# Optimization experiments

Measured on AMD Instinct MI355X. Metric: run time of the kernel, lower is better.

## Reference

```python
import jax, jax.numpy as jnp
import numpy as np

N, M, H = 200000, 400000, 128
EPS = 1e-12  # torch F.normalize eps


def _l2norm(x):
    # F.normalize(x, p=2, dim=-1): x / max(||x||, eps)
    n = jnp.linalg.norm(x, axis=-1, keepdims=True)
    return x / jnp.maximum(n, EPS)


def message_norm(feat, msg, scale):
    # DGL MessageNorm(learn_scale=True): normalize(msg) * ||feat|| * scale
    feat_norm = jnp.linalg.norm(feat, axis=-1, keepdims=True)
    return _l2norm(msg) * feat_norm * scale


def setup_inputs() -> dict:
    key = jax.random.key(0)
    ks = jax.random.split(key, 8)
    h_src = jax.random.normal(ks[0], (M, H), dtype=jnp.float32)
    c_src = jax.random.normal(ks[1], (M, H), dtype=jnp.float32)
    iou = jax.random.normal(ks[2], (N, 3 * H), dtype=jnp.float32)
    child_idx = jax.random.randint(ks[3], (N, 2), 0, M, dtype=jnp.int64)
    # torch nn.Linear layout: y = x @ W.T + b
    lim_f = 1.0 / np.sqrt(2 * H)
    W_f = jax.random.uniform(ks[4], (2 * H, 2 * H), minval=-lim_f, maxval=lim_f, dtype=jnp.float32)
    b_f = jax.random.uniform(ks[5], (2 * H,), minval=-lim_f, maxval=lim_f, dtype=jnp.float32)
    W_iou = jax.random.uniform(ks[6], (3 * H, 2 * H), minval=-lim_f, maxval=lim_f, dtype=jnp.float32)
    b_iou = jnp.zeros((1, 3 * H), dtype=jnp.float32)
    scale_iou = jnp.ones((), dtype=jnp.float32)
    scale_c = jnp.ones((), dtype=jnp.float32)
    return {"h_src": h_src, "c_src": c_src, "iou": iou, "child_idx": child_idx,
            "W_f": W_f, "b_f": b_f, "W_iou": W_iou, "b_iou": b_iou,
            "scale_iou": scale_iou, "scale_c": scale_c}


def reference(h_src, c_src, iou, child_idx, W_f, b_f, W_iou, b_iou, scale_iou, scale_c):
    # --- reduce_func: gather children, forget gates, weighted cell sum ---
    h_ch = h_src[child_idx]                 # [N, 2, H]
    c_ch = c_src[child_idx]                 # [N, 2, H]
    h_cat = h_ch.reshape(h_ch.shape[0], -1)  # [N, 2H]
    f = jax.nn.sigmoid(h_cat @ W_f.T + b_f).reshape(h_ch.shape)  # [N, 2, H]
    c_sum = jnp.sum(f * c_ch, axis=1)       # [N, H]
    iou_n = message_norm(iou, h_cat, scale_iou) @ W_iou.T  # [N, 3H]
    c_dat = message_norm(c_ch[:, 0, :], c_sum, scale_c)    # [N, H]
    # --- apply_node_func ---
    iou_b = iou_n + b_iou
    i, o, u = jnp.split(iou_b, 3, axis=1)
    c = jax.nn.sigmoid(i) * jnp.tanh(u) + c_dat
    h = jax.nn.sigmoid(o) * jnp.tanh(c)
    return jnp.stack([h, c], axis=1)        # [N, 2, H]
```

## Files before the change

kernel.cpp:

```cpp
#include <hip/hip_runtime.h>
#include <math.h>

typedef __attribute__((ext_vector_type(4))) float f32x4;
typedef __attribute__((ext_vector_type(2))) float f32x2;
typedef __attribute__((ext_vector_type(8))) short bf16x8;
typedef __attribute__((ext_vector_type(4))) short short4v;

#define EPSN 1e-12f
#define TN 32
#define FS 260
#define IS 388
#define FBASE 8192
#define UTOT 16512

__device__ inline short f2bf(float x) {
    union { float f; unsigned u; } v; v.f = x;
    unsigned r = v.u + 0x7fffu + ((v.u >> 16) & 1u);
    return (short)(r >> 16);
}
__device__ inline float bf2f(short s) {
    union { unsigned u; float f; } v;
    v.u = ((unsigned)(unsigned short)s) << 16;
    return v.f;
}
__device__ inline float wsum64(float v) {
#pragma unroll
    for (int m = 32; m > 0; m >>= 1) v += __shfl_xor(v, m);
    return v;
}
__device__ inline float wsum32(float v) {
    v += __shfl_xor(v, 1);
    v += __shfl_xor(v, 2);
    v += __shfl_xor(v, 4);
    v += __shfl_xor(v, 8);
    v += __shfl_xor(v, 16);
    return v;
}
__device__ inline float sigm(float x) { return 1.0f / (1.0f + __expf(-x)); }
__device__ inline float tanh_fast(float x) {
    float a = fabsf(x);
    float e = __expf(2.0f * a);
    float t = 1.0f - 2.0f / (e + 1.0f);
    return copysignf(t, x);
}
__device__ inline float dot4(f32x4 v) { return v.x*v.x + v.y*v.y + v.z*v.z + v.w*v.w; }
__device__ inline short4v pack4(f32x4 v) {
    short4v p;
    p.x = f2bf(v.x); p.y = f2bf(v.y); p.z = f2bf(v.z); p.w = f2bf(v.w);
    return p;
}

__global__ void prep_B(const float* __restrict__ W_f, const float* __restrict__ W_iou,
                       short* __restrict__ Blin) {
    int t = blockIdx.x * 256 + threadIdx.x;
    if (t >= 8 * 40 * 64) return;
    int lane = t & 63;
    int jb = (t >> 6) % 40;
    int kb = (t >> 6) / 40;
    int j = jb * 16 + (lane & 15);
    int k = kb * 32 + ((lane >> 4) << 3);
    const float* src = (j < 256) ? (W_f + (size_t)j * 256 + k)
                                 : (W_iou + (size_t)(j - 256) * 256 + k);
    bf16x8 v;
#pragma unroll
    for (int e = 0; e < 8; ++e) v[e] = f2bf(src[e]);
    *(bf16x8*)(Blin + (size_t)t * 8) = v;
}

template<int NJJ>
__device__ inline void gpass32(const short* __restrict__ A, const short* __restrict__ Blin,
                               int lane, int jbase, f32x4 acc[2][NJJ]) {
    const int la = lane & 15, kg = lane >> 4;
#pragma unroll
    for (int kb = 0; kb < 8; ++kb) {
        bf16x8 af[2];
#pragma unroll
        for (int m = 0; m < 2; ++m) {
            const int f = kb * 128 + kg * 32 + m * 16 + la;
            af[m] = *(const bf16x8*)&A[(f ^ ((f >> 5) & 7)) << 3];
        }
#pragma unroll
        for (int jj = 0; jj < NJJ; ++jj) {
            const bf16x8 b = *(const bf16x8*)(Blin +
                ((size_t)((kb * 40 + jbase + jj) * 64 + lane)) * 8);
            acc[0][jj] = __builtin_amdgcn_mfma_f32_16x16x32_bf16(af[0], b, acc[0][jj], 0, 0, 0);
            acc[1][jj] = __builtin_amdgcn_mfma_f32_16x16x32_bf16(af[1], b, acc[1][jj], 0, 0, 0);
        }
    }
}

__global__ __launch_bounds__(512, 4) void tree_fused(
    const float* __restrict__ h_src, const float* __restrict__ c_src,
    const float* __restrict__ iou, const int* __restrict__ child_idx,
    const float* __restrict__ b_f, const float* __restrict__ b_iou,
    const float* __restrict__ sc_iou_p, const float* __restrict__ sc_c_p,
    const short* __restrict__ Blin, float* __restrict__ out) {
    __shared__ __align__(16) short U[UTOT];
    __shared__ float h_n2[TN], iou_n2[TN];
    __shared__ int cc_lds[TN][2];

    const int tid = threadIdx.x;
    const int wave = tid >> 6;
    const int lane = tid & 63;
    const int la = lane & 15, kg = lane >> 4;
    const size_t nb0 = (size_t)blockIdx.x * TN;

    const float sc_iou = sc_iou_p[0];
    const float sc_c = sc_c_p[0];

    {
        const int child = lane >> 5;
        const int seg = lane & 31;
        int cix[4];
#pragma unroll
        for (int r = 0; r < 4; ++r)
            cix[r] = child_idx[(size_t)(nb0 + wave + 8 * r) * 2 + child];
#pragma unroll
        for (int half = 0; half < 2; ++half) {
            f32x4 hv[2], v4[2];
            f32x2 v2[2];
#pragma unroll
            for (int rr = 0; rr < 2; ++rr) {
                const int r = half * 2 + rr;
                const size_t node = nb0 + wave + 8 * r;
                hv[rr] = *(const f32x4*)(h_src + (size_t)cix[r] * 128 + seg * 4);
                v4[rr] = *(const f32x4*)(iou + node * 384 + lane * 4);
                v2[rr] = *(const f32x2*)(iou + node * 384 + 256 + lane * 2);
            }
#pragma unroll
            for (int rr = 0; rr < 2; ++rr) {
                const int r = half * 2 + rr;
                const int nd = wave + 8 * r;
                const int f = (child * 4 + (seg >> 3)) * 128 + ((seg >> 1) & 3) * 32 + nd;
                const int addr = ((f ^ ((f >> 5) & 7)) << 3) + (seg & 1) * 4;
                short4v a4;
                a4.x = f2bf(hv[rr].x); a4.y = f2bf(hv[rr].y);
                a4.z = f2bf(hv[rr].z); a4.w = f2bf(hv[rr].w);
                *(short4v*)&U[addr] = a4;
                if (lane == 0) cc_lds[nd][0] = cix[r];
                if (lane == 32) cc_lds[nd][1] = cix[r];
                float hss = wsum64(dot4(hv[rr]));
                float iss = wsum64(dot4(v4[rr]) + v2[rr].x * v2[rr].x + v2[rr].y * v2[rr].y);
                if (lane == 0) { h_n2[nd] = hss; iou_n2[nd] = iss; }
            }
            __builtin_amdgcn_sched_barrier(0);
        }
    }
    __syncthreads();

    const int nd0 = tid >> 5;
    const int q = tid & 31;
    const int h0q = q * 4;

    short4v c0a, c1a;
    float n2a;
    {
        const int c00 = cc_lds[nd0][0];
        const int c01 = cc_lds[nd0][1];
        const f32x4 t0 = *(const f32x4*)(c_src + (size_t)c00 * 128 + h0q);
        const f32x4 t1 = *(const f32x4*)(c_src + (size_t)c01 * 128 + h0q);
        n2a = dot4(t0);
        c0a = pack4(t0);
        c1a = pack4(t1);
    }

    {
        f32x4 accf[2][2];
        const float bf0 = b_f[(wave * 2 + 0) * 16 + la];
        const float bf1 = b_f[(wave * 2 + 1) * 16 + la];
        accf[0][0] = (f32x4){bf0, bf0, bf0, bf0};
        accf[1][0] = accf[0][0];
        accf[0][1] = (f32x4){bf1, bf1, bf1, bf1};
        accf[1][1] = accf[0][1];
        gpass32<2>(U, Blin, lane, wave * 2, accf);
#pragma unroll
        for (int m = 0; m < 2; ++m)
#pragma unroll
            for (int jj = 0; jj < 2; ++jj) {
                const int col = (wave * 2 + jj) * 16 + la;
#pragma unroll
                for (int r = 0; r < 4; ++r) {
                    const int row = m * 16 + kg * 4 + r;
                    U[FBASE + row * FS + col] = f2bf(accf[m][jj][r]);
                }
            }
    }

    short4v c0b, c1b;
    float n2b;
    {
        const int c10 = cc_lds[16 + nd0][0];
        const int c11 = cc_lds[16 + nd0][1];
        const f32x4 t0 = *(const f32x4*)(c_src + (size_t)c10 * 128 + h0q);
        const f32x4 t1 = *(const f32x4*)(c_src + (size_t)c11 * 128 + h0q);
        n2b = dot4(t0);
        c0b = pack4(t0);
        c1b = pack4(t1);
    }
    __syncthreads();

    f32x4 accio[2][3];
#pragma unroll
    for (int m = 0; m < 2; ++m)
#pragma unroll
        for (int jj = 0; jj < 3; ++jj) accio[m][jj] = (f32x4){0.f, 0.f, 0.f, 0.f};
    gpass32<3>(U, Blin, lane, 16 + wave * 3, accio);

    float csr[2][4], s_v[2];
#pragma unroll
    for (int p = 0; p < 2; ++p) {
        const int nd = p * 16 + nd0;
        const short4v c0v = p ? c0b : c0a;
        const short4v c1v = p ? c1b : c1a;
        const short4v yf0 = *(const short4v*)&U[FBASE + nd * FS + h0q];
        const short4v yf1 = *(const short4v*)&U[FBASE + nd * FS + 128 + h0q];
        float c0n2 = wsum32(p ? n2b : n2a);
        float cs[4];
        float csn2 = 0.f;
#pragma unroll
        for (int e = 0; e < 4; ++e) {
            const float f0 = sigm(bf2f(yf0[e]));
            const float f1 = sigm(bf2f(yf1[e]));
            const float v = f0 * bf2f(c0v[e]) + f1 * bf2f(c1v[e]);
            cs[e] = v;
            csn2 += v * v;
        }
        csn2 = wsum32(csn2);
        const float rs = sc_c * sqrtf(c0n2) / fmaxf(sqrtf(csn2), EPSN);
#pragma unroll
        for (int e = 0; e < 4; ++e) csr[p][e] = cs[e] * rs;
        s_v[p] = sc_iou * sqrtf(iou_n2[nd]) / fmaxf(sqrtf(h_n2[nd]), EPSN);
    }
    __syncthreads();

#pragma unroll
    for (int m = 0; m < 2; ++m)
#pragma unroll
        for (int jj = 0; jj < 3; ++jj) {
            const int col = (wave * 3 + jj) * 16 + la;
#pragma unroll
            for (int r = 0; r < 4; ++r) {
                const int row = m * 16 + kg * 4 + r;
                U[row * IS + col] = f2bf(accio[m][jj][r]);
            }
        }
    __syncthreads();

    const f32x4 bi0 = *(const f32x4*)(b_iou + h0q);
    const f32x4 bi1 = *(const f32x4*)(b_iou + 128 + h0q);
    const f32x4 bi2 = *(const f32x4*)(b_iou + 256 + h0q);
#pragma unroll
    for (int p = 0; p < 2; ++p) {
        const int nd = p * 16 + nd0;
        const size_t node = nb0 + nd;
        const short4v yi = *(const short4v*)&U[nd * IS + h0q];
        const short4v yo = *(const short4v*)&U[nd * IS + 128 + h0q];
        const short4v yu = *(const short4v*)&U[nd * IS + 256 + h0q];
        f32x4 outh, outc;
#pragma unroll
        for (int e = 0; e < 4; ++e) {
            const float iv = bf2f(yi[e]) * s_v[p] + ((const float*)&bi0)[e];
            const float ov = bf2f(yo[e]) * s_v[p] + ((const float*)&bi1)[e];
            const float uv = bf2f(yu[e]) * s_v[p] + ((const float*)&bi2)[e];
            const float cval = sigm(iv) * tanh_fast(uv) + csr[p][e];
            const float hval = sigm(ov) * tanh_fast(cval);
            ((float*)&outh)[e] = hval;
            ((float*)&outc)[e] = cval;
        }
        *(f32x4*)(out + node * 256 + h0q) = outh;
        *(f32x4*)(out + node * 256 + 128 + h0q) = outc;
    }
}

extern "C" void kernel_launch(void* const* d_in, const int* in_sizes, int n_in,
                              void* d_out, int out_size, void* d_ws, size_t ws_size,
                              hipStream_t stream) {
    const float* h_src = (const float*)d_in[0];
    const float* c_src = (const float*)d_in[1];
    const float* iou = (const float*)d_in[2];
    const int* cidx = (const int*)d_in[3];
    const float* W_f = (const float*)d_in[4];
    const float* b_f = (const float*)d_in[5];
    const float* W_iou = (const float*)d_in[6];
    const float* b_iou = (const float*)d_in[7];
    const float* s_iou = (const float*)d_in[8];
    const float* s_c = (const float*)d_in[9];
    float* out = (float*)d_out;
    short* Blin = (short*)d_ws;

    const int N = in_sizes[3] / 2;
    const int ntiles = N / TN;
    hipLaunchKernelGGL(prep_B, dim3(80), dim3(256), 0, stream, W_f, W_iou, Blin);
    hipLaunchKernelGGL(tree_fused, dim3(ntiles), dim3(512), 0, stream,
                       h_src, c_src, iou, cidx, b_f, b_iou, s_iou, s_c, Blin, out);
}
```

Baseline: 255.2 us.

## Make tree kernel persistent with double-buffered prefetch of next tile's gathers

Converts the one-tile-per-block kernel into a persistent grid-stride loop over 512 blocks, double-buffering the A-operand tile, child indices and norms in LDS. Gathers and norms for the next tile are issued while the current tile's GEMMs and epilogue run, so gather latency overlaps with compute. LDS use grows to about 74 KB per block, which lowers occupancy (the grid is capped at 512 blocks) and adds register pressure from the prefetched values held across the loop.

After: 616.8 us. +141.6%, slower.

```diff
diff --git a/kernel.cpp b/kernel.cpp
--- a/kernel.cpp
+++ b/kernel.cpp
@@ -8,10 +8,13 @@
 
 #define EPSN 1e-12f
 #define TN 32
-#define FS 260
-#define IS 388
-#define FBASE 8192
-#define UTOT 16512
+#define A1B 8192
+#define FB  16384
+#define FS  260
+#define IOB 24704
+#define IS  388
+#define UTOT 37120
+#define NBLK 512
 
 __device__ inline short f2bf(float x) {
     union { float f; unsigned u; } v; v.f = x;
@@ -94,27 +97,40 @@
     const float* __restrict__ iou, const int* __restrict__ child_idx,
     const float* __restrict__ b_f, const float* __restrict__ b_iou,
     const float* __restrict__ sc_iou_p, const float* __restrict__ sc_c_p,
-    const short* __restrict__ Blin, float* __restrict__ out) {
+    const short* __restrict__ Blin, float* __restrict__ out, int ntiles) {
     __shared__ __align__(16) short U[UTOT];
-    __shared__ float h_n2[TN], iou_n2[TN];
-    __shared__ int cc_lds[TN][2];
+    __shared__ float h_n2[2][TN], iou_n2[2][TN];
+    __shared__ int cc_lds[2][TN][2];
 
     const int tid = threadIdx.x;
     const int wave = tid >> 6;
     const int lane = tid & 63;
     const int la = lane & 15, kg = lane >> 4;
-    const size_t nb0 = (size_t)blockIdx.x * TN;
+    const int G = gridDim.x;
 
     const float sc_iou = sc_iou_p[0];
     const float sc_c = sc_c_p[0];
 
+    const int child = lane >> 5;
+    const int seg = lane & 31;
+
+    const int nd0 = tid >> 5;
+    const int q = tid & 31;
+    const int h0q = q * 4;
+
+    const float bf0 = b_f[(wave * 2 + 0) * 16 + la];
+    const float bf1 = b_f[(wave * 2 + 1) * 16 + la];
+
+    const int t0 = blockIdx.x;
+    if (t0 >= ntiles) return;
+
+    int idxA[4];
+
     {
-        const int child = lane >> 5;
-        const int seg = lane & 31;
         int cix[4];
 #pragma unroll
         for (int r = 0; r < 4; ++r)
-            cix[r] = child_idx[(size_t)(nb0 + wave + 8 * r) * 2 + child];
+            cix[r] = child_idx[(size_t)(t0 * TN + wave + 8 * r) * 2 + child];
 #pragma unroll
         for (int half = 0; half < 2; ++half) {
             f32x4 hv[2], v4[2];
@@ -122,7 +138,7 @@
 #pragma unroll
             for (int rr = 0; rr < 2; ++rr) {
                 const int r = half * 2 + rr;
-                const size_t node = nb0 + wave + 8 * r;
+                const size_t node = (size_t)t0 * TN + wave + 8 * r;
                 hv[rr] = *(const f32x4*)(h_src + (size_t)cix[r] * 128 + seg * 4);
                 v4[rr] = *(const f32x4*)(iou + node * 384 + lane * 4);
                 v2[rr] = *(const f32x2*)(iou + node * 384 + 256 + lane * 2);
@@ -133,142 +149,188 @@
                 const int nd = wave + 8 * r;
                 const int f = (child * 4 + (seg >> 3)) * 128 + ((seg >> 1) & 3) * 32 + nd;
                 const int addr = ((f ^ ((f >> 5) & 7)) << 3) + (seg & 1) * 4;
-                short4v a4;
-                a4.x = f2bf(hv[rr].x); a4.y = f2bf(hv[rr].y);
-                a4.z = f2bf(hv[rr].z); a4.w = f2bf(hv[rr].w);
-                *(short4v*)&U[addr] = a4;
-                if (lane == 0) cc_lds[nd][0] = cix[r];
-                if (lane == 32) cc_lds[nd][1] = cix[r];
+                *(short4v*)&U[addr] = pack4(hv[rr]);
+                if (lane == 0) cc_lds[0][nd][0] = cix[r];
+                if (lane == 32) cc_lds[0][nd][1] = cix[r];
                 float hss = wsum64(dot4(hv[rr]));
                 float iss = wsum64(dot4(v4[rr]) + v2[rr].x * v2[rr].x + v2[rr].y * v2[rr].y);
-                if (lane == 0) { h_n2[nd] = hss; iou_n2[nd] = iss; }
+                if (lane == 0) { h_n2[0][nd] = hss; iou_n2[0][nd] = iss; }
             }
             __builtin_amdgcn_sched_barrier(0);
+        }
+        if (t0 + G < ntiles) {
+#pragma unroll
+            for (int r = 0; r < 4; ++r)
+                idxA[r] = child_idx[(size_t)((t0 + G) * TN + wave + 8 * r) * 2 + child];
         }
     }
     __syncthreads();
 
-    const int nd0 = tid >> 5;
-    const int q = tid & 31;
-    const int h0q = q * 4;
-
-    short4v c0a, c1a;
-    float n2a;
-    {
-        const int c00 = cc_lds[nd0][0];
-        const int c01 = cc_lds[nd0][1];
-        const f32x4 t0 = *(const f32x4*)(c_src + (size_t)c00 * 128 + h0q);
-        const f32x4 t1 = *(const f32x4*)(c_src + (size_t)c01 * 128 + h0q);
-        n2a = dot4(t0);
-        c0a = pack4(t0);
-        c1a = pack4(t1);
-    }
-
-    {
-        f32x4 accf[2][2];
-        const float bf0 = b_f[(wave * 2 + 0) * 16 + la];
-        const float bf1 = b_f[(wave * 2 + 1) * 16 + la];
-        accf[0][0] = (f32x4){bf0, bf0, bf0, bf0};
-        accf[1][0] = accf[0][0];
-        accf[0][1] = (f32x4){bf1, bf1, bf1, bf1};
-        accf[1][1] = accf[0][1];
-        gpass32<2>(U, Blin, lane, wave * 2, accf);
-#pragma unroll
-        for (int m = 0; m < 2; ++m)
-#pragma unroll
-            for (int jj = 0; jj < 2; ++jj) {
-                const int col = (wave * 2 + jj) * 16 + la;
-#pragma unroll
-                for (int r = 0; r < 4; ++r) {
-                    const int row = m * 16 + kg * 4 + r;
-                    U[FBASE + row * FS + col] = f2bf(accf[m][jj][r]);
-                }
-            }
-    }
-
-    short4v c0b, c1b;
-    float n2b;
-    {
-        const int c10 = cc_lds[16 + nd0][0];
-        const int c11 = cc_lds[16 + nd0][1];
-        const f32x4 t0 = *(const f32x4*)(c_src + (size_t)c10 * 128 + h0q);
-        const f32x4 t1 = *(const f32x4*)(c_src + (size_t)c11 * 128 + h0q);
-        n2b = dot4(t0);
-        c0b = pack4(t0);
-        c1b = pack4(t1);
-    }
-    __syncthreads();
-
-    f32x4 accio[2][3];
-#pragma unroll
-    for (int m = 0; m < 2; ++m)
-#pragma unroll
-        for (int jj = 0; jj < 3; ++jj) accio[m][jj] = (f32x4){0.f, 0.f, 0.f, 0.f};
-    gpass32<3>(U, Blin, lane, 16 + wave * 3, accio);
-
-    float csr[2][4], s_v[2];
-#pragma unroll
-    for (int p = 0; p < 2; ++p) {
-        const int nd = p * 16 + nd0;
-        const short4v c0v = p ? c0b : c0a;
-        const short4v c1v = p ? c1b : c1a;
-        const short4v yf0 = *(const short4v*)&U[FBASE + nd * FS + h0q];
-        const short4v yf1 = *(const short4v*)&U[FBASE + nd * FS + 128 + h0q];
-        float c0n2 = wsum32(p ? n2b : n2a);
-        float cs[4];
-        float csn2 = 0.f;
-#pragma unroll
-        for (int e = 0; e < 4; ++e) {
-            const float f0 = sigm(bf2f(yf0[e]));
-            const float f1 = sigm(bf2f(yf1[e]));
-            const float v = f0 * bf2f(c0v[e]) + f1 * bf2f(c1v[e]);
-            cs[e] = v;
-            csn2 += v * v;
-        }
-        csn2 = wsum32(csn2);
-        const float rs = sc_c * sqrtf(c0n2) / fmaxf(sqrtf(csn2), EPSN);
-#pragma unroll
-        for (int e = 0; e < 4; ++e) csr[p][e] = cs[e] * rs;
-        s_v[p] = sc_iou * sqrtf(iou_n2[nd]) / fmaxf(sqrtf(h_n2[nd]), EPSN);
-    }
-    __syncthreads();
-
-#pragma unroll
-    for (int m = 0; m < 2; ++m)
-#pragma unroll
-        for (int jj = 0; jj < 3; ++jj) {
-            const int col = (wave * 3 + jj) * 16 + la;
-#pragma unroll
-            for (int r = 0; r < 4; ++r) {
-                const int row = m * 16 + kg * 4 + r;
-                U[row * IS + col] = f2bf(accio[m][jj][r]);
-            }
-        }
-    __syncthreads();
-
-    const f32x4 bi0 = *(const f32x4*)(b_iou + h0q);
-    const f32x4 bi1 = *(const f32x4*)(b_iou + 128 + h0q);
-    const f32x4 bi2 = *(const f32x4*)(b_iou + 256 + h0q);
-#pragma unroll
-    for (int p = 0; p < 2; ++p) {
-        const int nd = p * 16 + nd0;
-        const size_t node = nb0 + nd;
-        const short4v yi = *(const short4v*)&U[nd * IS + h0q];
-        const short4v yo = *(const short4v*)&U[nd * IS + 128 + h0q];
-        const short4v yu = *(const short4v*)&U[nd * IS + 256 + h0q];
-        f32x4 outh, outc;
-#pragma unroll
-        for (int e = 0; e < 4; ++e) {
-            const float iv = bf2f(yi[e]) * s_v[p] + ((const float*)&bi0)[e];
-            const float ov = bf2f(yo[e]) * s_v[p] + ((const float*)&bi1)[e];
-            const float uv = bf2f(yu[e]) * s_v[p] + ((const float*)&bi2)[e];
-            const float cval = sigm(iv) * tanh_fast(uv) + csr[p][e];
-            const float hval = sigm(ov) * tanh_fast(cval);
-            ((float*)&outh)[e] = hval;
-            ((float*)&outc)[e] = cval;
-        }
-        *(f32x4*)(out + node * 256 + h0q) = outh;
-        *(f32x4*)(out + node * 256 + 128 + h0q) = outc;
+    int b = 0;
+    for (int t = t0; t < ntiles; t += G, b ^= 1) {
+        const int nt = t + G;
+        const bool hn = nt < ntiles;
+        const int Ab = b * A1B;
+        const int An = A1B - Ab;
+
+        f32x4 hvn[4];
+        if (hn) {
+#pragma unroll
+            for (int r = 0; r < 4; ++r)
+                hvn[r] = *(const f32x4*)(h_src + (size_t)idxA[r] * 128 + seg * 4);
+        }
+
+        short4v c0a, c1a;
+        float n2a;
+        {
+            const int c00 = cc_lds[b][nd0][0];
+            const int c01 = cc_lds[b][nd0][1];
+            const f32x4 p0 = *(const f32x4*)(c_src + (size_t)c00 * 128 + h0q);
+            const f32x4 p1 = *(const f32x4*)(c_src + (size_t)c01 * 128 + h0q);
+            n2a = dot4(p0);
+            c0a = pack4(p0);
+            c1a = pack4(p1);
+        }
+
+        {
+            f32x4 accf[2][2];
+            accf[0][0] = (f32x4){bf0, bf0, bf0, bf0};
+            accf[1][0] = accf[0][0];
+            accf[0][1] = (f32x4){bf1, bf1, bf1, bf1};
+            accf[1][1] = accf[0][1];
+            gpass32<2>(&U[Ab], Blin, lane, wave * 2, accf);
+#pragma unroll
+            for (int m = 0; m < 2; ++m)
+#pragma unroll
+                for (int jj = 0; jj < 2; ++jj) {
+                    const int col = (wave * 2 + jj) * 16 + la;
+#pragma unroll
+                    for (int r = 0; r < 4; ++r) {
+                        const int row = m * 16 + kg * 4 + r;
+                        U[FB + row * FS + col] = f2bf(accf[m][jj][r]);
+                    }
+                }
+        }
+
+        short4v c0b, c1b;
+        float n2b;
+        {
+            const int c10 = cc_lds[b][16 + nd0][0];
+            const int c11 = cc_lds[b][16 + nd0][1];
+            const f32x4 p0 = *(const f32x4*)(c_src + (size_t)c10 * 128 + h0q);
+            const f32x4 p1 = *(const f32x4*)(c_src + (size_t)c11 * 128 + h0q);
+            n2b = dot4(p0);
+            c0b = pack4(p0);
+            c1b = pack4(p1);
+        }
+        __syncthreads();
+
+        float csr[2][4], s_v[2];
+#pragma unroll
+        for (int p = 0; p < 2; ++p) {
+            const int nd = p * 16 + nd0;
+            const short4v c0v = p ? c0b : c0a;
+            const short4v c1v = p ? c1b : c1a;
+            const short4v yf0 = *(const short4v*)&U[FB + nd * FS + h0q];
+            const short4v yf1 = *(const short4v*)&U[FB + nd * FS + 128 + h0q];
+            float c0n2 = wsum32(p ? n2b : n2a);
+            float cs[4];
+            float csn2 = 0.f;
+#pragma unroll
+            for (int e = 0; e < 4; ++e) {
+                const float f0 = sigm(bf2f(yf0[e]));
+                const float f1 = sigm(bf2f(yf1[e]));
+                const float v = f0 * bf2f(c0v[e]) + f1 * bf2f(c1v[e]);
+                cs[e] = v;
+                csn2 += v * v;
+            }
+            csn2 = wsum32(csn2);
+            const float rs = sc_c * sqrtf(c0n2) / fmaxf(sqrtf(csn2), EPSN);
+#pragma unroll
+            for (int e = 0; e < 4; ++e) csr[p][e] = cs[e] * rs;
+            s_v[p] = sc_iou * sqrtf(iou_n2[b][nd]) / fmaxf(sqrtf(h_n2[b][nd]), EPSN);
+        }
+
+        if (hn) {
+#pragma unroll
+            for (int half = 0; half < 2; ++half) {
+                f32x4 v4[2];
+                f32x2 v2[2];
+#pragma unroll
+                for (int rr = 0; rr < 2; ++rr) {
+                    const int r = half * 2 + rr;
+                    const size_t node = (size_t)nt * TN + wave + 8 * r;
+                    v4[rr] = *(const f32x4*)(iou + node * 384 + lane * 4);
+                    v2[rr] = *(const f32x2*)(iou + node * 384 + 256 + lane * 2);
+                }
+#pragma unroll
+                for (int rr = 0; rr < 2; ++rr) {
+                    const int r = half * 2 + rr;
+                    const int nd = wave + 8 * r;
+                    const int f = (child * 4 + (seg >> 3)) * 128 + ((seg >> 1) & 3) * 32 + nd;
+                    const int addr = An + ((f ^ ((f >> 5) & 7)) << 3) + (seg & 1) * 4;
+                    *(short4v*)&U[addr] = pack4(hvn[r]);
+                    if (lane == 0) cc_lds[b ^ 1][nd][0] = idxA[r];
+                    if (lane == 32) cc_lds[b ^ 1][nd][1] = idxA[r];
+                    float hss = wsum64(dot4(hvn[r]));
+                    float iss = wsum64(dot4(v4[rr]) + v2[rr].x * v2[rr].x + v2[rr].y * v2[rr].y);
+                    if (lane == 0) { h_n2[b ^ 1][nd] = hss; iou_n2[b ^ 1][nd] = iss; }
+                }
+            }
+        }
+        if (nt + G < ntiles) {
+#pragma unroll
+            for (int r = 0; r < 4; ++r)
+                idxA[r] = child_idx[(size_t)((nt + G) * TN + wave + 8 * r) * 2 + child];
+        }
+
+        {
+            f32x4 accio[2][3];
+#pragma unroll
+            for (int m = 0; m < 2; ++m)
+#pragma unroll
+                for (int jj = 0; jj < 3; ++jj) accio[m][jj] = (f32x4){0.f, 0.f, 0.f, 0.f};
+            gpass32<3>(&U[Ab], Blin, lane, 16 + wave * 3, accio);
+#pragma unroll
+            for (int m = 0; m < 2; ++m)
+#pragma unroll
+                for (int jj = 0; jj < 3; ++jj) {
+                    const int col = (wave * 3 + jj) * 16 + la;
+#pragma unroll
+                    for (int r = 0; r < 4; ++r) {
+                        const int row = m * 16 + kg * 4 + r;
+                        U[IOB + row * IS + col] = f2bf(accio[m][jj][r]);
+                    }
+                }
+        }
+        __syncthreads();
+
+        {
+            const f32x4 bi0 = *(const f32x4*)(b_iou + h0q);
+            const f32x4 bi1 = *(const f32x4*)(b_iou + 128 + h0q);
+            const f32x4 bi2 = *(const f32x4*)(b_iou + 256 + h0q);
+#pragma unroll
+            for (int p = 0; p < 2; ++p) {
+                const int nd = p * 16 + nd0;
+                const size_t node = (size_t)t * TN + nd;
+                const short4v yi = *(const short4v*)&U[IOB + nd * IS + h0q];
+                const short4v yo = *(const short4v*)&U[IOB + nd * IS + 128 + h0q];
+                const short4v yu = *(const short4v*)&U[IOB + nd * IS + 256 + h0q];
+                f32x4 outh, outc;
+#pragma unroll
+                for (int e = 0; e < 4; ++e) {
+                    const float iv = bf2f(yi[e]) * s_v[p] + ((const float*)&bi0)[e];
+                    const float ov = bf2f(yo[e]) * s_v[p] + ((const float*)&bi1)[e];
+                    const float uv = bf2f(yu[e]) * s_v[p] + ((const float*)&bi2)[e];
+                    const float cval = sigm(iv) * tanh_fast(uv) + csr[p][e];
+                    const float hval = sigm(ov) * tanh_fast(cval);
+                    ((float*)&outh)[e] = hval;
+                    ((float*)&outc)[e] = cval;
+                }
+                *(f32x4*)(out + node * 256 + h0q) = outh;
+                *(f32x4*)(out + node * 256 + 128 + h0q) = outc;
+            }
+        }
     }
 }
 
@@ -290,7 +352,8 @@
 
     const int N = in_sizes[3] / 2;
     const int ntiles = N / TN;
+    const int grid = (ntiles < NBLK) ? ntiles : NBLK;
     hipLaunchKernelGGL(prep_B, dim3(80), dim3(256), 0, stream, W_f, W_iou, Blin);
-    hipLaunchKernelGGL(tree_fused, dim3(ntiles), dim3(512), 0, stream,
-                       h_src, c_src, iou, cidx, b_f, b_iou, s_iou, s_c, Blin, out);
-}
+    hipLaunchKernelGGL(tree_fused, dim3(grid), dim3(512), 0, stream,
+                       h_src, c_src, iou, cidx, b_f, b_iou, s_iou, s_c, Blin, out, ntiles);
+}
```

## Give iou GEMM output its own LDS region and drop two block barriers

Applied to the files above, without the earlier changes.

The iou GEMM result now goes to a separate LDS region (IOB) instead of reusing the input tile area, so it can be written right after the GEMM without waiting for other waves to finish reading the inputs. This removes two __syncthreads and merges the forget-gate epilogue with the final gate epilogue. All four c_src gathers are also issued up front so their latency overlaps the forget GEMM. In exchange LDS use per block grows, which may lower occupancy.

Measured after the change: 264.0 us. +3.4%, slower.

```diff
diff --git a/kernel.cpp b/kernel.cpp
--- a/kernel.cpp
+++ b/kernel.cpp
@@ -11,7 +11,8 @@
 #define FS 260
 #define IS 388
 #define FBASE 8192
-#define UTOT 16512
+#define IOB 16512
+#define UTOT 28928
 
 __device__ inline short f2bf(float x) {
     union { float f; unsigned u; } v; v.f = x;
@@ -133,10 +134,7 @@
                 const int nd = wave + 8 * r;
                 const int f = (child * 4 + (seg >> 3)) * 128 + ((seg >> 1) & 3) * 32 + nd;
                 const int addr = ((f ^ ((f >> 5) & 7)) << 3) + (seg & 1) * 4;
-                short4v a4;
-                a4.x = f2bf(hv[rr].x); a4.y = f2bf(hv[rr].y);
-                a4.z = f2bf(hv[rr].z); a4.w = f2bf(hv[rr].w);
-                *(short4v*)&U[addr] = a4;
+                *(short4v*)&U[addr] = pack4(hv[rr]);
                 if (lane == 0) cc_lds[nd][0] = cix[r];
                 if (lane == 32) cc_lds[nd][1] = cix[r];
                 float hss = wsum64(dot4(hv[rr]));
@@ -152,16 +150,21 @@
     const int q = tid & 31;
     const int h0q = q * 4;
 
-    short4v c0a, c1a;
-    float n2a;
+    short4v c0a, c1a, c0b, c1b;
+    float n2a, n2b;
     {
         const int c00 = cc_lds[nd0][0];
         const int c01 = cc_lds[nd0][1];
+        const int c10 = cc_lds[16 + nd0][0];
+        const int c11 = cc_lds[16 + nd0][1];
         const f32x4 t0 = *(const f32x4*)(c_src + (size_t)c00 * 128 + h0q);
         const f32x4 t1 = *(const f32x4*)(c_src + (size_t)c01 * 128 + h0q);
+        const f32x4 t2 = *(const f32x4*)(c_src + (size_t)c10 * 128 + h0q);
+        const f32x4 t3 = *(const f32x4*)(c_src + (size_t)c11 * 128 + h0q);
         n2a = dot4(t0);
-        c0a = pack4(t0);
-        c1a = pack4(t1);
+        n2b = dot4(t2);
+        c0a = pack4(t0); c1a = pack4(t1);
+        c0b = pack4(t2); c1b = pack4(t3);
     }
 
     {
@@ -186,30 +189,34 @@
             }
     }
 
-    short4v c0b, c1b;
-    float n2b;
-    {
-        const int c10 = cc_lds[16 + nd0][0];
-        const int c11 = cc_lds[16 + nd0][1];
-        const f32x4 t0 = *(const f32x4*)(c_src + (size_t)c10 * 128 + h0q);
-        const f32x4 t1 = *(const f32x4*)(c_src + (size_t)c11 * 128 + h0q);
-        n2b = dot4(t0);
-        c0b = pack4(t0);
-        c1b = pack4(t1);
+    {
+        f32x4 accio[2][3];
+#pragma unroll
+        for (int m = 0; m < 2; ++m)
+#pragma unroll
+            for (int jj = 0; jj < 3; ++jj) accio[m][jj] = (f32x4){0.f, 0.f, 0.f, 0.f};
+        gpass32<3>(U, Blin, lane, 16 + wave * 3, accio);
+#pragma unroll
+        for (int m = 0; m < 2; ++m)
+#pragma unroll
+            for (int jj = 0; jj < 3; ++jj) {
+                const int col = (wave * 3 + jj) * 16 + la;
+#pragma unroll
+                for (int r = 0; r < 4; ++r) {
+                    const int row = m * 16 + kg * 4 + r;
+                    U[IOB + row * IS + col] = f2bf(accio[m][jj][r]);
+                }
+            }
     }
     __syncthreads();
 
-    f32x4 accio[2][3];
-#pragma unroll
-    for (int m = 0; m < 2; ++m)
-#pragma unroll
-        for (int jj = 0; jj < 3; ++jj) accio[m][jj] = (f32x4){0.f, 0.f, 0.f, 0.f};
-    gpass32<3>(U, Blin, lane, 16 + wave * 3, accio);
-
-    float csr[2][4], s_v[2];
+    const f32x4 bi0 = *(const f32x4*)(b_iou + h0q);
+    const f32x4 bi1 = *(const f32x4*)(b_iou + 128 + h0q);
+    const f32x4 bi2 = *(const f32x4*)(b_iou + 256 + h0q);
 #pragma unroll
     for (int p = 0; p < 2; ++p) {
         const int nd = p * 16 + nd0;
+        const size_t node = nb0 + nd;
         const short4v c0v = p ? c0b : c0a;
         const short4v c1v = p ? c1b : c1a;
         const short4v yf0 = *(const short4v*)&U[FBASE + nd * FS + h0q];
@@ -227,42 +234,18 @@
         }
         csn2 = wsum32(csn2);
         const float rs = sc_c * sqrtf(c0n2) / fmaxf(sqrtf(csn2), EPSN);
-#pragma unroll
-        for (int e = 0; e < 4; ++e) csr[p][e] = cs[e] * rs;
-        s_v[p] = sc_iou * sqrtf(iou_n2[nd]) / fmaxf(sqrtf(h_n2[nd]), EPSN);
-    }
-    __syncthreads();
-
-#pragma unroll
-    for (int m = 0; m < 2; ++m)
-#pragma unroll
-        for (int jj = 0; jj < 3; ++jj) {
-            const int col = (wave * 3 + jj) * 16 + la;
-#pragma unroll
-            for (int r = 0; r < 4; ++r) {
-                const int row = m * 16 + kg * 4 + r;
-                U[row * IS + col] = f2bf(accio[m][jj][r]);
-            }
-        }
-    __syncthreads();
-
-    const f32x4 bi0 = *(const f32x4*)(b_iou + h0q);
-    const f32x4 bi1 = *(const f32x4*)(b_iou + 128 + h0q);
-    const f32x4 bi2 = *(const f32x4*)(b_iou + 256 + h0q);
-#pragma unroll
-    for (int p = 0; p < 2; ++p) {
-        const int nd = p * 16 + nd0;
-        const size_t node = nb0 + nd;
-        const short4v yi = *(const short4v*)&U[nd * IS + h0q];
-        const short4v yo = *(const short4v*)&U[nd * IS + 128 + h0q];
-        const short4v yu = *(const short4v*)&U[nd * IS + 256 + h0q];
+        const float s_v = sc_iou * sqrtf(iou_n2[nd]) / fmaxf(sqrtf(h_n2[nd]), EPSN);
+
+        const short4v yi = *(const short4v*)&U[IOB + nd * IS + h0q];
+        const short4v yo = *(const short4v*)&U[IOB + nd * IS + 128 + h0q];
+        const short4v yu = *(const short4v*)&U[IOB + nd * IS + 256 + h0q];
         f32x4 outh, outc;
 #pragma unroll
         for (int e = 0; e < 4; ++e) {
-            const float iv = bf2f(yi[e]) * s_v[p] + ((const float*)&bi0)[e];
-            const float ov = bf2f(yo[e]) * s_v[p] + ((const float*)&bi1)[e];
-            const float uv = bf2f(yu[e]) * s_v[p] + ((const float*)&bi2)[e];
-            const float cval = sigm(iv) * tanh_fast(uv) + csr[p][e];
+            const float iv = bf2f(yi[e]) * s_v + ((const float*)&bi0)[e];
+            const float ov = bf2f(yo[e]) * s_v + ((const float*)&bi1)[e];
+            const float uv = bf2f(yu[e]) * s_v + ((const float*)&bi2)[e];
+            const float cval = sigm(iv) * tanh_fast(uv) + cs[e] * rs;
             const float hval = sigm(ov) * tanh_fast(cval);
             ((float*)&outh)[e] = hval;
             ((float*)&outc)[e] = cval;
```
